# Optimization experiments

Measured on AMD Instinct MI355X. Metric: run time of the kernel, lower is better.

## Reference

```python
import jax, jax.numpy as jnp
import numpy as np

B, N, M, D = 2, 16384, 2048, 256
LN_EPS = 1e-5


def setup_inputs() -> dict:
    key = jax.random.key(0)
    ks = jax.random.split(key, 12)
    inv = 1.0 / np.sqrt(D)
    return {
        "p_xyz": jax.random.normal(ks[0], (B, N, 3), jnp.float32),
        "v_xyz": jax.random.normal(ks[1], (B, 3), jnp.float32),
        "p_features": jax.random.normal(ks[2], (B, N, D), jnp.float32),
        "v_features": jax.random.normal(ks[3], (B, M, D), jnp.float32),
        "Wq": jax.random.normal(ks[4], (D, D), jnp.float32) * inv,
        "bq": jnp.zeros((D,), jnp.float32),
        "Wk": jax.random.normal(ks[5], (D, D), jnp.float32) * inv,
        "bk": jnp.zeros((D,), jnp.float32),
        "Wv": jax.random.normal(ks[6], (D, D), jnp.float32) * inv,
        "bv": jnp.zeros((D,), jnp.float32),
        "Wp1": jax.random.normal(ks[7], (3, 3), jnp.float32) * (1.0 / np.sqrt(3.0)),
        "bp1": jnp.zeros((3,), jnp.float32),
        "ln_w": jnp.ones((3,), jnp.float32),
        "ln_b": jnp.zeros((3,), jnp.float32),
        "Wp2": jax.random.normal(ks[8], (3, D), jnp.float32) * (1.0 / np.sqrt(3.0)),
        "bp2": jnp.zeros((D,), jnp.float32),
    }


def reference(p_xyz, v_xyz, p_features, v_features,
              Wq, bq, Wk, bk, Wv, bv,
              Wp1, bp1, ln_w, ln_b, Wp2, bp2):
    d_model = Wq.shape[1]
    # dist: [B, N, 3] = |p_xyz - v_xyz| (v_xyz broadcast over N)
    dist = jnp.abs(p_xyz - v_xyz[:, None, :])
    # fc_p: Linear(3,3) -> LayerNorm(3) -> ReLU -> Linear(3, d_model)
    h = dist @ Wp1 + bp1                                   # [B, N, 3]
    mu = jnp.mean(h, axis=-1, keepdims=True)
    var = jnp.mean((h - mu) ** 2, axis=-1, keepdims=True)
    h = (h - mu) / jnp.sqrt(var + LN_EPS) * ln_w + ln_b
    pv = jax.nn.relu(h) @ Wp2 + bp2                        # [B, N, D]

    q = v_features @ Wq + bq                               # [B, M, D]
    k = p_features @ Wk + bk                               # [B, N, D]
    v = p_features @ Wv + bv                               # [B, N, D]

    # q@k^T + q@pv^T == q @ (k+pv)^T, scaled by sqrt(d_model)
    scale = 1.0 / jnp.sqrt(jnp.asarray(d_model, q.dtype))
    logits = jnp.einsum('bmd,bnd->bmn', q, k + pv) * scale  # [B, M, N]
    w = jax.nn.softmax(logits, axis=-2)                     # softmax over M (dim=-2)
    res = jnp.einsum('bmn,bnd->bmd', w, v)                  # [B, M, D]
    return res + v_features
```

## Files before the change

### kernel.cpp

```cpp
#include <hip/hip_runtime.h>
#include <math.h>

namespace {

constexpr int   B_ = 2;
constexpr int   N_ = 16384;
constexpr int   M_ = 2048;
constexpr int   D_ = 256;
constexpr float QS_ = 0.09016844005556021f;
constexpr float LN_EPS_ = 1e-5f;
constexpr int   NS_  = 16;
constexpr int   NPB_ = N_ / NS_;
constexpr int   NCOPY_ = 8;
constexpr int   NT16_ = N_ / 16;
constexpr int   MT32_ = M_ / 32;
constexpr size_t OUTSZ_ = (size_t)B_*M_*D_;

typedef _Float16 f16x8 __attribute__((ext_vector_type(8)));
typedef float    f32x16 __attribute__((ext_vector_type(16)));
typedef unsigned int u32x2 __attribute__((ext_vector_type(2)));

__device__ inline f16x8 as_h8(uint4 u) { return __builtin_bit_cast(f16x8, u); }
__device__ inline unsigned short f16bits(float x) {
    return __builtin_bit_cast(unsigned short, (_Float16)x);
}
__device__ inline unsigned int pack2(float a, float b) {
    return (unsigned int)f16bits(a) | ((unsigned int)f16bits(b) << 16);
}
__device__ inline uint4 pack8(const unsigned short v[8]) {
    return make_uint4((uint32_t)v[0] | ((uint32_t)v[1] << 16),
                      (uint32_t)v[2] | ((uint32_t)v[3] << 16),
                      (uint32_t)v[4] | ((uint32_t)v[5] << 16),
                      (uint32_t)v[6] | ((uint32_t)v[7] << 16));
}
#define MFMA16(acc, a, b) (acc) = __builtin_amdgcn_mfma_f32_32x32x16_f16((a), (b), (acc), 0, 0, 0)

__device__ inline int cd_row(int reg, int lane) {
    return (reg & 3) + 8 * (reg >> 2) + 4 * (lane >> 5);
}

__device__ inline size_t SP(int bloc, int g16, int tm) {
    return (((size_t)bloc * NT16_ + g16) * MT32_ + tm) * 64;
}

__global__ void prep_wt(const float* __restrict__ Wq, const float* __restrict__ Wk,
                        const float* __restrict__ Wv, uint4* __restrict__ wp) {
    __shared__ unsigned short ldb[256 * 33];
    const int mat = blockIdx.x >> 3;
    const int Tc  = blockIdx.x & 7;
    const float* W = (mat == 0) ? Wq : (mat == 1) ? Wk : Wv;
    const float scl = (mat == 0) ? QS_ : 1.0f;
    const int d = threadIdx.x;
    #pragma unroll
    for (int c = 0; c < 32; c += 4) {
        const float4 v = *reinterpret_cast<const float4*>(&W[d * D_ + Tc * 32 + c]);
        ldb[d * 33 + c + 0] = f16bits(v.x * scl);
        ldb[d * 33 + c + 1] = f16bits(v.y * scl);
        ldb[d * 33 + c + 2] = f16bits(v.z * scl);
        ldb[d * 33 + c + 3] = f16bits(v.w * scl);
    }
    __syncthreads();
    const int lane = threadIdx.x & 63;
    const int pg   = threadIdx.x >> 6;
    #pragma unroll
    for (int kq = 0; kq < 4; ++kq) {
        const int ks = pg * 4 + kq;
        unsigned short hh[8];
        #pragma unroll
        for (int j = 0; j < 8; ++j)
            hh[j] = ldb[(ks * 16 + (lane >> 5) * 8 + j) * 33 + (lane & 31)];
        wp[((size_t)((mat * 8 + Tc) * 16 + ks)) * 64 + lane] = pack8(hh);
    }
}

__global__ void prep_hr(const float* __restrict__ p_xyz, const float* __restrict__ v_xyz,
                        const float* __restrict__ Wp1, const float* __restrict__ bp1,
                        const float* __restrict__ ln_w, const float* __restrict__ ln_b,
                        float4* __restrict__ hr4) {
    const int r = blockIdx.x * 256 + threadIdx.x;
    if (r >= B_ * N_) return;
    const int b = r / N_;
    const float d0 = fabsf(p_xyz[r*3+0] - v_xyz[b*3+0]);
    const float d1 = fabsf(p_xyz[r*3+1] - v_xyz[b*3+1]);
    const float d2 = fabsf(p_xyz[r*3+2] - v_xyz[b*3+2]);
    float h[3];
    #pragma unroll
    for (int j = 0; j < 3; ++j)
        h[j] = d0*Wp1[0*3+j] + d1*Wp1[1*3+j] + d2*Wp1[2*3+j] + bp1[j];
    const float mu = (h[0]+h[1]+h[2]) * (1.0f/3.0f);
    const float e0 = h[0]-mu, e1 = h[1]-mu, e2 = h[2]-mu;
    const float var = (e0*e0 + e1*e1 + e2*e2) * (1.0f/3.0f);
    const float inv = rsqrtf(var + LN_EPS_);
    hr4[r] = make_float4(fmaxf(e0*inv*ln_w[0] + ln_b[0], 0.0f),
                         fmaxf(e1*inv*ln_w[1] + ln_b[1], 0.0f),
                         fmaxf(e2*inv*ln_w[2] + ln_b[2], 0.0f), 0.0f);
}

template<int MODE>
__global__ void gemm_qkv(const float* __restrict__ in,
                         const uint4* __restrict__ wp,
                         const float* __restrict__ bias,
                         const float4* __restrict__ hr4,
                         const float* __restrict__ Wp2, const float* __restrict__ bp2,
                         const float* __restrict__ sc, int roff32,
                         uint4* __restrict__ op) {
    __shared__ unsigned short tb[4][32 * 33];
    __shared__ float scb[64];
    const int tid  = threadIdx.x;
    const int lane = tid & 63;
    const int w    = tid >> 6;
    const int wr   = w & 1;
    const int wc   = w >> 1;
    const int lane31 = lane & 31;
    const int Trow = roff32 + blockIdx.x * 2 + wr;
    const int rowA = Trow * 32 + lane31;
    const float* ap = in + (size_t)rowA * D_ + (lane >> 5) * 8;

    if (MODE == 2) {
        if (tid < 64) scb[tid] = sc[(roff32 + blockIdx.x * 2) * 32 + tid];
        __syncthreads();
    }

    f32x16 acc[4];
    #pragma unroll
    for (int t = 0; t < 4; ++t) acc[t] = (f32x16)0.0f;

    union U8 { _Float16 f[8]; f16x8 v; };
    #pragma unroll 4
    for (int ks = 0; ks < 16; ++ks) {
        const float4 f0 = *reinterpret_cast<const float4*>(ap + ks*16);
        const float4 f1 = *reinterpret_cast<const float4*>(ap + ks*16 + 4);
        const float xs[8] = {f0.x, f0.y, f0.z, f0.w, f1.x, f1.y, f1.z, f1.w};
        U8 ah, al;
        #pragma unroll
        for (int j = 0; j < 8; ++j) {
            ah.f[j] = (_Float16)xs[j];
            al.f[j] = (_Float16)(xs[j] - (float)ah.f[j]);
        }
        #pragma unroll
        for (int t = 0; t < 4; ++t) {
            const f16x8 bh = as_h8(wp[((size_t)((wc * 4 + t) * 16 + ks)) * 64 + lane]);
            MFMA16(acc[t], ah.v, bh);
            MFMA16(acc[t], al.v, bh);
        }
    }

    const float bscale = (MODE == 0) ? QS_ : 1.0f;
    float biasc[4], w0c[4], w1c[4], w2c[4], b2c[4];
    #pragma unroll
    for (int t = 0; t < 4; ++t) {
        const int cc = wc * 128 + t * 32 + lane31;
        biasc[t] = bias[cc] * bscale;
        if (MODE == 1) {
            w0c[t] = Wp2[0*D_ + cc]; w1c[t] = Wp2[1*D_ + cc];
            w2c[t] = Wp2[2*D_ + cc]; b2c[t] = bp2[cc];
        }
    }
    float4 hv[16];
    if (MODE == 1) {
        #pragma unroll
        for (int r = 0; r < 16; ++r) hv[r] = hr4[Trow * 32 + cd_row(r, lane)];
    }

    #pragma unroll
    for (int t = 0; t < 4; ++t) {
        #pragma unroll
        for (int r = 0; r < 16; ++r) {
            float v = acc[t][r] + biasc[t];
            if (MODE == 1) v += hv[r].x*w0c[t] + hv[r].y*w1c[t] + hv[r].z*w2c[t] + b2c[t];
            if (MODE == 2) v *= scb[wr * 32 + cd_row(r, lane)];
            tb[w][cd_row(r, lane) * 33 + lane31] = f16bits(v);
        }
        if (MODE != 2) {
            #pragma unroll
            for (int p = 0; p < 2; ++p) {
                unsigned short hh[8];
                #pragma unroll
                for (int j = 0; j < 8; ++j)
                    hh[j] = tb[w][lane31 * 33 + p * 16 + (lane >> 5) * 8 + j];
                op[((size_t)(Trow * 16 + wc * 8 + t * 2 + p)) * 64 + lane] = pack8(hh);
            }
        } else {
            #pragma unroll
            for (int h16 = 0; h16 < 2; ++h16) {
                unsigned short hh[8];
                #pragma unroll
                for (int j = 0; j < 8; ++j)
                    hh[j] = tb[w][(h16 * 16 + (lane >> 5) * 8 + j) * 33 + lane31];
                op[((size_t)((Trow * 2 + h16) * 8 + wc * 4 + t)) * 64 + lane] = pack8(hh);
            }
        }
    }
}

template<int NB>
__global__ __launch_bounds__(256, 2)
void sgemm(const uint4* __restrict__ qp, const uint4* __restrict__ kp,
           uint4* __restrict__ sws, float* __restrict__ t0p, int b0) {
    const int tid  = threadIdx.x;
    const int lane = tid & 63;
    const int w    = tid >> 6;
    const int g    = blockIdx.x * 4 + w;
    const int mh   = g & 1;
    const int r    = g >> 1;
    const int bl   = (NB == 2) ? (r & 1) : 0;
    const int n32  = (NB == 2) ? (r >> 1) : r;
    const int b    = b0 + bl;
    const int Tn   = b * (N_ / 32) + n32;

    uint4 kf[16];
    #pragma unroll
    for (int ks = 0; ks < 16; ++ks)
        kf[ks] = kp[((size_t)(Tn * 16 + ks)) * 64 + lane];

    float tacc[16];
    #pragma unroll
    for (int q = 0; q < 16; ++q) tacc[q] = 0.0f;

    for (int t = 0; t < 32; ++t) {
        const int Tm = mh * 32 + t;
        uint4 qa[16];
        #pragma unroll
        for (int ks = 0; ks < 16; ++ks)
            qa[ks] = qp[((size_t)((b * MT32_ + Tm) * 16 + ks)) * 64 + lane];
        f32x16 sT0 = (f32x16)0.0f, sT1 = (f32x16)0.0f;
        #pragma unroll
        for (int ks = 0; ks < 16; ks += 2) {
            MFMA16(sT0, as_h8(kf[ks]),   as_h8(qa[ks]));
            MFMA16(sT1, as_h8(kf[ks+1]), as_h8(qa[ks+1]));
        }
        float ee[16];
        #pragma unroll
        for (int q = 0; q < 16; ++q) {
            ee[q] = exp2f(fminf(sT0[q] + sT1[q], 15.5f));
            tacc[q] += ee[q];
        }
        unsigned int pk[8];
        #pragma unroll
        for (int i = 0; i < 8; ++i) pk[i] = pack2(ee[2*i], ee[2*i+1]);
        const u32x2 r0 = __builtin_amdgcn_permlane32_swap(pk[0], pk[2], false, false);
        const u32x2 r1 = __builtin_amdgcn_permlane32_swap(pk[1], pk[3], false, false);
        const u32x2 r2 = __builtin_amdgcn_permlane32_swap(pk[4], pk[6], false, false);
        const u32x2 r3 = __builtin_amdgcn_permlane32_swap(pk[5], pk[7], false, false);
        sws[SP(bl, n32 * 2 + 0, Tm) + lane] = make_uint4(r0[0], r1[0], r0[1], r1[1]);
        sws[SP(bl, n32 * 2 + 1, Tm) + lane] = make_uint4(r2[0], r3[0], r2[1], r3[1]);
    }

    #pragma unroll
    for (int q = 0; q < 16; ++q) {
        #pragma unroll
        for (int off = 16; off; off >>= 1)
            tacc[q] += __shfl_xor(tacc[q], off, 64);
    }
    if ((lane & 31) == 0) {
        #pragma unroll
        for (int q = 0; q < 16; ++q) {
            const int n = n32 * 32 + cd_row(q, lane);
            t0p[((size_t)(mh * B_ + b)) * N_ + n] = tacc[q];
        }
    }
}

__global__ void calc_sc(const float* __restrict__ t0p, float* __restrict__ sc, int b0) {
    const int b = b0 + blockIdx.x;
    const int tid = threadIdx.x;
    const float4* p0 = (const float4*)(t0p + ((size_t)(0 * B_ + b)) * N_);
    const float4* p1 = (const float4*)(t0p + ((size_t)(1 * B_ + b)) * N_);
    float4* s4 = (float4*)(sc + (size_t)b * N_);
    for (int i = tid; i < N_/4; i += 256) {
        const float4 a = p0[i], c = p1[i];
        float4 o;
        o.x = fminf(1.0f / (a.x + c.x), 60000.0f);
        o.y = fminf(1.0f / (a.y + c.y), 60000.0f);
        o.z = fminf(1.0f / (a.z + c.z), 60000.0f);
        o.w = fminf(1.0f / (a.w + c.w), 60000.0f);
        s4[i] = o;
    }
}

template<int NB>
__global__ __launch_bounds__(256, 3)
void attn_out(const uint4* __restrict__ sws, const uint4* __restrict__ vp,
              float* __restrict__ part, int b0) {
    const int tid  = threadIdx.x;
    const int lane = tid & 63;
    const int w    = tid >> 6;
    const int wm   = w & 1;
    const int wd   = w >> 1;
    const int lane31 = lane & 31;

    const int bid  = blockIdx.x;
    const int low3 = bid & 7;
    const int rest = bid >> 3;
    const int g    = (rest & (2*NB - 1)) * 8 + low3;
    const int bl   = g >> 4;
    const int b    = b0 + bl;
    const int ns   = g & 15;
    const int mt   = rest >> (NB == 2 ? 2 : 1);
    const int m0   = mt * 64;
    const int TmG  = mt * 2 + wm;

    f32x16 oacc[4];
    #pragma unroll
    for (int t = 0; t < 4; ++t) oacc[t] = (f32x16)0.0f;

    #pragma unroll 2
    for (int c = 0; c < NPB_ / 64; ++c) {
        const int nbase = ns * NPB_ + c * 64;
        const int g16   = nbase >> 4;
        uint4 af[4];
        #pragma unroll
        for (int t = 0; t < 4; ++t)
            af[t] = sws[SP(bl, g16 + t, TmG) + lane];
        const size_t gg0 = (size_t)((b * N_ + nbase) >> 4);
        #pragma unroll
        for (int k2 = 0; k2 < 4; ++k2) {
            #pragma unroll
            for (int dt = 0; dt < 4; ++dt) {
                MFMA16(oacc[dt], as_h8(af[k2]),
                       as_h8(vp[((gg0 + k2) * 8 + wd * 4 + dt) * 64 + lane]));
            }
        }
    }
    float* pb = part + (size_t)low3 * OUTSZ_;
    #pragma unroll
    for (int dt = 0; dt < 4; ++dt) {
        #pragma unroll
        for (int r = 0; r < 16; ++r) {
            const int row = m0 + wm * 32 + cd_row(r, lane);
            atomicAdd(&pb[((size_t)(b * M_ + row)) * D_ + wd * 128 + dt * 32 + lane31],
                      oacc[dt][r]);
        }
    }
}

__global__ void reduce_out(const float4* __restrict__ v, const float4* __restrict__ part,
                           float4* __restrict__ out) {
    const size_t i = (size_t)blockIdx.x * 256 + threadIdx.x;
    float4 a = v[i];
    #pragma unroll
    for (int c = 0; c < NCOPY_; ++c) {
        const float4 p = part[(size_t)c * (OUTSZ_ / 4) + i];
        a.x += p.x; a.y += p.y; a.z += p.z; a.w += p.w;
    }
    out[i] = a;
}

}

extern "C" void kernel_launch(void* const* d_in, const int* in_sizes, int n_in,
                              void* d_out, int out_size, void* d_ws, size_t ws_size,
                              hipStream_t stream) {
    const float* p_xyz      = (const float*)d_in[0];
    const float* v_xyz      = (const float*)d_in[1];
    const float* p_features = (const float*)d_in[2];
    const float* v_features = (const float*)d_in[3];
    const float* Wq  = (const float*)d_in[4];
    const float* bq  = (const float*)d_in[5];
    const float* Wk  = (const float*)d_in[6];
    const float* bk  = (const float*)d_in[7];
    const float* Wv  = (const float*)d_in[8];
    const float* bv  = (const float*)d_in[9];
    const float* Wp1 = (const float*)d_in[10];
    const float* bp1 = (const float*)d_in[11];
    const float* lnw = (const float*)d_in[12];
    const float* lnb = (const float*)d_in[13];
    const float* Wp2 = (const float*)d_in[14];
    const float* bp2 = (const float*)d_in[15];
    float* out = (float*)d_out;

    char* p = (char*)d_ws;
    auto alloc = [&](size_t bytes) {
        void* r = (void*)p;
        p += (bytes + 255) & ~(size_t)255;
        return r;
    };
    uint4* qpk = (uint4*)alloc((size_t)B_*M_*D_*2);
    uint4* kpk = (uint4*)alloc((size_t)B_*N_*D_*2);
    uint4* vpk = (uint4*)alloc((size_t)B_*N_*D_*2);
    uint4* wp  = (uint4*)alloc((size_t)3*D_*D_*2);
    float4* hr4 = (float4*)alloc((size_t)B_*N_*16);
    float*  t0p = (float*)alloc((size_t)2*B_*N_*4);
    float*  sc  = (float*)alloc((size_t)B_*N_*4);
    float*  part = (float*)alloc((size_t)NCOPY_*OUTSZ_*4);

    const size_t swsFull = (size_t)B_ * M_ * N_ * 2;
    const size_t used = (size_t)(p - (char*)d_ws);
    const bool full = ws_size >= used + swsFull;
    uint4* sws = (uint4*)alloc(full ? swsFull : swsFull / 2);

    constexpr size_t WMAT = (size_t)D_*D_/8;

    prep_wt<<<3*8, 256, 0, stream>>>(Wq, Wk, Wv, wp);
    prep_hr<<<(B_*N_)/256, 256, 0, stream>>>(p_xyz, v_xyz, Wp1, bp1, lnw, lnb, hr4);
    hipMemsetAsync(part, 0, (size_t)NCOPY_*OUTSZ_*4, stream);

    gemm_qkv<0><<<(B_*M_)/64, 256, 0, stream>>>(v_features, wp + 0*WMAT, bq, hr4, Wp2, bp2, nullptr, 0, qpk);
    gemm_qkv<1><<<(B_*N_)/64, 256, 0, stream>>>(p_features, wp + 1*WMAT, bk, hr4, Wp2, bp2, nullptr, 0, kpk);

    if (full) {
        sgemm<2><<<512, 256, 0, stream>>>(qpk, kpk, sws, t0p, 0);
        calc_sc<<<2, 256, 0, stream>>>(t0p, sc, 0);
        gemm_qkv<2><<<(B_*N_)/64, 256, 0, stream>>>(p_features, wp + 2*WMAT, bv, hr4, Wp2, bp2, sc, 0, vpk);
        attn_out<2><<<8*4*32, 256, 0, stream>>>(sws, vpk, part, 0);
    } else {
        for (int b = 0; b < B_; ++b) {
            sgemm<1><<<256, 256, 0, stream>>>(qpk, kpk, sws, t0p, b);
            calc_sc<<<1, 256, 0, stream>>>(t0p, sc, b);
            gemm_qkv<2><<<N_/64, 256, 0, stream>>>(p_features, wp + 2*WMAT, bv, hr4, Wp2, bp2, sc,
                                                   b * (N_/32), vpk);
            attn_out<1><<<8*2*32, 256, 0, stream>>>(sws, vpk, part, b);
        }
    }
    reduce_out<<<(OUTSZ_/4)/256, 256, 0, stream>>>((const float4*)v_features,
                                                   (const float4*)part, (float4*)out);
}
```

Baseline: 374.1 us.

## Stage attn_out operand tiles through double-buffered LDS shared across waves

```diff
diff --git a/kernel.cpp b/kernel.cpp
--- a/kernel.cpp
+++ b/kernel.cpp
@@ -279,9 +279,10 @@
 }
 
 template<int NB>
-__global__ __launch_bounds__(256, 3)
+__global__ __launch_bounds__(256, 4)
 void attn_out(const uint4* __restrict__ sws, const uint4* __restrict__ vp,
               float* __restrict__ part, int b0) {
+    __shared__ uint4 lds[2][1280];
     const int tid  = threadIdx.x;
     const int lane = tid & 63;
     const int w    = tid >> 6;
@@ -298,30 +299,57 @@
     const int ns   = g & 15;
     const int mt   = rest >> (NB == 2 ? 2 : 1);
     const int m0   = mt * 64;
-    const int TmG  = mt * 2 + wm;
+
+    const int nb0  = ns * NPB_;
+    const size_t gg0 = (size_t)((b * N_ + nb0) >> 4);
+    const int g16_0  = nb0 >> 4;
+    const uint4* gsrc[5];
+    int dsti[5];
+    int gstep[5];
+    #pragma unroll
+    for (int j = 0; j < 5; ++j) {
+        const int f = w * 5 + j;
+        if (f < 16) {
+            gsrc[j]  = vp + (gg0 * 8 + f) * 64 + lane;
+            dsti[j]  = f * 64 + lane;
+            gstep[j] = 2 * 8 * 64;
+        } else {
+            const int pi = f - 16;
+            gsrc[j]  = sws + SP(bl, g16_0 + (pi & 1), mt * 2 + (pi >> 1)) + lane;
+            dsti[j]  = 1024 + pi * 64 + lane;
+            gstep[j] = 2 * MT32_ * 64;
+        }
+    }
 
     f32x16 oacc[4];
     #pragma unroll
     for (int t = 0; t < 4; ++t) oacc[t] = (f32x16)0.0f;
 
+    uint4 st[5];
+    #pragma unroll
+    for (int j = 0; j < 5; ++j) { st[j] = *gsrc[j]; gsrc[j] += gstep[j]; }
+
+    constexpr int NCH = NPB_ / 32;
     #pragma unroll 2
-    for (int c = 0; c < NPB_ / 64; ++c) {
-        const int nbase = ns * NPB_ + c * 64;
-        const int g16   = nbase >> 4;
-        uint4 af[4];
-        #pragma unroll
-        for (int t = 0; t < 4; ++t)
-            af[t] = sws[SP(bl, g16 + t, TmG) + lane];
-        const size_t gg0 = (size_t)((b * N_ + nbase) >> 4);
-        #pragma unroll
-        for (int k2 = 0; k2 < 4; ++k2) {
+    for (int c = 0; c < NCH; ++c) {
+        uint4* Bf = lds[c & 1];
+        #pragma unroll
+        for (int j = 0; j < 5; ++j) Bf[dsti[j]] = st[j];
+        if (c < NCH - 1) {
+            #pragma unroll
+            for (int j = 0; j < 5; ++j) { st[j] = *gsrc[j]; gsrc[j] += gstep[j]; }
+        }
+        asm volatile("s_waitcnt lgkmcnt(0)\n\ts_barrier" ::: "memory");
+        #pragma unroll
+        for (int k2 = 0; k2 < 2; ++k2) {
+            const f16x8 af = as_h8(Bf[1024 + (k2 + 2 * wm) * 64 + lane]);
             #pragma unroll
             for (int dt = 0; dt < 4; ++dt) {
-                MFMA16(oacc[dt], as_h8(af[k2]),
-                       as_h8(vp[((gg0 + k2) * 8 + wd * 4 + dt) * 64 + lane]));
+                MFMA16(oacc[dt], af, as_h8(Bf[(k2 * 8 + wd * 4 + dt) * 64 + lane]));
             }
         }
     }
+
     float* pb = part + (size_t)low3 * OUTSZ_;
     #pragma unroll
     for (int dt = 0; dt < 4; ++dt) {
```

Result: slower. 480.3 us (+28.4%).
